# Kernel tuning notes

Hardware: AMD Instinct MI355X
Metric: run time of the kernel (lower is better)

## Reference

```python
import jax, jax.numpy as jnp
import numpy as np

B, T, C = 1, 4096, 1024   # batch, seq, n_embd
E, K = 64, 8              # num_experts, router top-k
G, TG = 8, 4              # n_group, topk_group
H, HS = 512, 2048         # expert hidden, shared-expert hidden
STD = 0.02


def setup_inputs() -> dict:
    key = jax.random.key(0)
    ks = jax.random.split(key, 9)
    return {
        "x": jax.random.normal(ks[0], (B, T, C), jnp.float32),
        "router_w": jax.random.normal(ks[1], (E, C), jnp.float32) * (C ** -0.5),
        "e_bias": jnp.zeros((E,), jnp.float32),  # e_score_correction_bias buffer
        "gate_w": jax.random.normal(ks[2], (E, C, H), jnp.float32) * STD,
        "up_w": jax.random.normal(ks[3], (E, C, H), jnp.float32) * STD,
        "down_w": jax.random.normal(ks[4], (E, H, C), jnp.float32) * STD,
        "sh_gate_w": jax.random.normal(ks[5], (C, HS), jnp.float32) * STD,
        "sh_up_w": jax.random.normal(ks[6], (C, HS), jnp.float32) * STD,
        "sh_down_w": jax.random.normal(ks[7], (HS, C), jnp.float32) * STD,
    }


def _route(xf, router_w, e_bias):
    # grouped sigmoid top-k routing with score-correction bias (group_limited_greedy)
    S = xf.shape[0]
    scores = jax.nn.sigmoid(xf @ router_w.T)          # [S,E], raw sigmoid scores
    sb = scores + e_bias                               # biased scores (selection only)
    epg = E // G
    # per-group score = sum of top (K // topk_group) biased scores in that group
    grp = jax.lax.top_k(sb.reshape(S, G, epg), K // TG)[0].sum(-1)   # [S,G]
    gidx = jax.lax.top_k(grp, TG)[1]                                 # [S,TG]
    gmask = jnp.zeros((S, G), bool).at[jnp.arange(S)[:, None], gidx].set(True)
    emask = jnp.repeat(gmask, epg, axis=1)                           # [S,E]
    masked = jnp.where(emask, sb, -jnp.inf)
    topk_idx = jax.lax.top_k(masked, K)[1]                           # [S,K]
    w = jnp.take_along_axis(scores, topk_idx, axis=1)                # raw scores gathered
    w = w / (w.sum(-1, keepdims=True) + 1e-20)                       # norm_topk_prob
    return topk_idx, w


def reference(x, router_w, e_bias, gate_w, up_w, down_w, sh_gate_w, sh_up_w, sh_down_w):
    Bq, Tq, Cq = x.shape
    xf = x.reshape(Bq * Tq, Cq)
    # always-on shared expert (SwiGLU)
    shared = (jax.nn.silu(xf @ sh_gate_w) * (xf @ sh_up_w)) @ sh_down_w
    topk_idx, w = _route(xf, router_w, e_bias)
    fe = topk_idx.reshape(-1)                          # [S*K] expert id per routed row
    order = jnp.argsort(fe, stable=True)               # sort rows by expert (grouped)
    tok = order // K                                   # source token of each sorted row
    sorted_x = xf[tok]                                 # [S*K, C]
    group_sizes = jnp.bincount(fe, length=E).astype(jnp.int32)
    # grouped GEMMs (== torch._grouped_mm / bmm-over-buckets in the original)
    g = jax.lax.ragged_dot(sorted_x, gate_w, group_sizes)
    u = jax.lax.ragged_dot(sorted_x, up_w, group_sizes)
    h = jax.nn.silu(g) * u
    o = jax.lax.ragged_dot(h, down_w, group_sizes)     # [S*K, C]
    o = o * w.reshape(-1)[order][:, None]              # weight by routing prob
    routed = jnp.zeros_like(xf).at[tok].add(o)         # combine back per token
    return (shared + routed).reshape(Bq, Tq, Cq)
```

## Files before the change

### kernel.cpp

```cpp
#include <hip/hip_runtime.h>
#include <hip/hip_bf16.h>
#include <stdint.h>


#define S_TOK 4096
#define C_DIM 1024
#define E_NUM 64
#define H_DIM 512
#define HS_DIM 2048
#define ROWS_TOTAL (S_TOK * 8)
#define T_TILES 320
#define NB_ROUTED_F (T_TILES * 8)
#define NB_SHARED_F (32 * 32)
#define NB_ROUTED_D (T_TILES * 8)
#define NB_SHARED_D (32 * 8)

typedef __attribute__((ext_vector_type(8))) short short8;
typedef __attribute__((ext_vector_type(4))) float f32x4;
typedef __attribute__((ext_vector_type(2))) unsigned int uint2v;

static __device__ __forceinline__ unsigned short f2bf(float f) {
    union { float f; uint32_t u; } v; v.f = f;
    uint32_t u = v.u;
    u += 0x7fffu + ((u >> 16) & 1u);
    return (unsigned short)(u >> 16);
}

static __device__ __forceinline__ void gl2lds16(const void* g, void* l) {
    __builtin_amdgcn_global_load_lds(
        (const __attribute__((address_space(1))) uint32_t*)g,
        (__attribute__((address_space(3))) uint32_t*)l, 16, 0, 0);
}

static __device__ __forceinline__ uint2v tr64(unsigned addr) {
    uint2v r;
    asm volatile("ds_read_b64_tr_b16 %0, %1" : "=v"(r) : "v"(addr));
    return r;
}

__global__ __launch_bounds__(256)
void router_scores_k(const float* __restrict__ x, const float* __restrict__ rw,
                     float* __restrict__ scores, int* __restrict__ counts) {
    if (blockIdx.x == 0 && threadIdx.x < E_NUM) counts[threadIdx.x] = 0;
    int t0 = blockIdx.x * 32;
    __shared__ float xs[32][36];
    __shared__ float wsm[64][36];
    int t = threadIdx.x;
    int tx = t & 15, ty = t >> 4;
    float acc[2][4] = {};
    for (int k0 = 0; k0 < C_DIM; k0 += 32) {
        {
            int r = t >> 3, c = t & 7;
            *(float4*)&xs[r][c * 4] = *(const float4*)(x + (size_t)(t0 + r) * C_DIM + k0 + c * 4);
        }
        #pragma unroll
        for (int i = 0; i < 2; i++) {
            int idx = t + 256 * i;
            int r = idx >> 3, c = idx & 7;
            *(float4*)&wsm[r][c * 4] = *(const float4*)(rw + (size_t)r * C_DIM + k0 + c * 4);
        }
        __syncthreads();
        #pragma unroll
        for (int kk = 0; kk < 32; kk += 4) {
            float4 a0 = *(const float4*)&xs[ty * 2 + 0][kk];
            float4 a1 = *(const float4*)&xs[ty * 2 + 1][kk];
            #pragma unroll
            for (int j = 0; j < 4; j++) {
                float4 b = *(const float4*)&wsm[tx * 4 + j][kk];
                acc[0][j] += a0.x * b.x + a0.y * b.y + a0.z * b.z + a0.w * b.w;
                acc[1][j] += a1.x * b.x + a1.y * b.y + a1.z * b.z + a1.w * b.w;
            }
        }
        __syncthreads();
    }
    #pragma unroll
    for (int i = 0; i < 2; i++)
        #pragma unroll
        for (int j = 0; j < 4; j++)
            scores[(size_t)(t0 + ty * 2 + i) * E_NUM + tx * 4 + j] =
                1.f / (1.f + __expf(-acc[i][j]));
}

__global__ __launch_bounds__(256)
void topk_k(const float* __restrict__ scores, const float* __restrict__ ebias,
            int* __restrict__ topk_idx, float* __restrict__ topk_w,
            int* __restrict__ counts) {
    int t = blockIdx.x * 4 + (threadIdx.x >> 6);
    int e = threadIdx.x & 63;
    float sc = scores[(size_t)t * E_NUM + e];
    float sb = sc + ebias[e];
    float m1 = sb, m2 = -1e30f;
    #pragma unroll
    for (int off = 1; off <= 4; off <<= 1) {
        float o1 = __shfl_xor(m1, off);
        float o2 = __shfl_xor(m2, off);
        float hi = fmaxf(m1, o1), lo = fminf(m1, o1);
        m2 = fmaxf(lo, fmaxf(m2, o2));
        m1 = hi;
    }
    float grp = m1 + m2;
    float grpv[8];
    #pragma unroll
    for (int g = 0; g < 8; g++) grpv[g] = __shfl(grp, g * 8);
    unsigned gsel = 0;
    #pragma unroll
    for (int k = 0; k < 4; k++) {
        float best = -1e30f; int bi = 0;
        #pragma unroll
        for (int g = 0; g < 8; g++)
            if (!((gsel >> g) & 1) && grpv[g] > best) { best = grpv[g]; bi = g; }
        gsel |= 1u << bi;
    }
    float val = ((gsel >> (e >> 3)) & 1) ? sb : -1e30f;
    int idx[8]; float sv[8]; float wsum = 0.f;
    #pragma unroll
    for (int k = 0; k < 8; k++) {
        uint32_t u = __float_as_uint(val);
        uint32_t mu = (u & 0x80000000u) ? ~u : (u | 0x80000000u);
        unsigned long long key = ((unsigned long long)mu << 6) | (unsigned long long)(63 - e);
        #pragma unroll
        for (int off = 32; off; off >>= 1) {
            unsigned long long ok = __shfl_xor(key, off);
            if (ok > key) key = ok;
        }
        int win = 63 - (int)(key & 63ull);
        idx[k] = win;
        sv[k] = __shfl(sc, win);
        wsum += sv[k];
        if (e == win) val = -1e30f;
    }
    float inv = 1.f / (wsum + 1e-20f);
    if (e < 8) {
        topk_idx[t * 8 + e] = idx[e];
        topk_w[t * 8 + e] = sv[e] * inv;
        atomicAdd(&counts[idx[e]], 1);
    }
}

__global__ void scan_k(const int* __restrict__ counts, int* __restrict__ base,
                       int* __restrict__ cursor, int* __restrict__ tile_e,
                       int* __restrict__ tile_m0) {
    int e = threadIdx.x;
    int c = counts[e];
    int s = c;
    #pragma unroll
    for (int off = 1; off < 64; off <<= 1) {
        int o = __shfl_up(s, off);
        if (e >= off) s += o;
    }
    int ex = s - c;
    base[e] = ex;
    cursor[e] = ex;
    int nt = (c + 127) >> 7;
    int ts = nt;
    #pragma unroll
    for (int off = 1; off < 64; off <<= 1) {
        int o = __shfl_up(ts, off);
        if (e >= off) ts += o;
    }
    int tb = ts - nt;
    for (int i = 0; i < nt; i++) { tile_e[tb + i] = e; tile_m0[tb + i] = i * 128; }
    int total = __shfl(ts, 63);
    for (int j = total + e; j < T_TILES; j += 64) tile_e[j] = -1;
}

__global__ void scatter_k(const int* __restrict__ topk_idx, const float* __restrict__ topk_w,
                          int* __restrict__ cursor, int* __restrict__ row_token,
                          float* __restrict__ row_wgt, int* __restrict__ pos_of) {
    int i = blockIdx.x * blockDim.x + threadIdx.x;
    int e = topk_idx[i];
    int pos = atomicAdd(&cursor[e], 1);
    row_token[pos] = i >> 3;
    row_wgt[pos] = topk_w[i];
    pos_of[i] = pos;
}

__global__ __launch_bounds__(256)
void combine_k(const float* __restrict__ O, const int* __restrict__ pos_of,
               float* __restrict__ out) {
    int t = blockIdx.x;
    int c = threadIdx.x;
    float4 s = ((const float4*)(out + (size_t)t * C_DIM))[c];
    int p[8];
    #pragma unroll
    for (int k = 0; k < 8; k++) p[k] = pos_of[t * 8 + k];
    #pragma unroll
    for (int k = 0; k < 8; k++) {
        float4 v = ((const float4*)(O + (size_t)p[k] * C_DIM))[c];
        s.x += v.x; s.y += v.y; s.z += v.z; s.w += v.w;
    }
    ((float4*)(out + (size_t)t * C_DIM))[c] = s;
}

__global__ __launch_bounds__(256)
void cvt_all_k(const float* __restrict__ i0, unsigned short* __restrict__ o0, int n0,
               const float* __restrict__ i1, unsigned short* __restrict__ o1, int n1,
               const float* __restrict__ i2, unsigned short* __restrict__ o2, int n2,
               const float* __restrict__ i3, unsigned short* __restrict__ o3, int n3,
               const float* __restrict__ i4, unsigned short* __restrict__ o4, int n4,
               const float* __restrict__ i5, unsigned short* __restrict__ o5, int n5,
               const float* __restrict__ i6, unsigned short* __restrict__ o6, int n6) {
    int g = blockIdx.x * 256 + threadIdx.x;
    const float* in; unsigned short* out;
    if (g < n0) { in = i0; out = o0; }
    else { g -= n0;
    if (g < n1) { in = i1; out = o1; }
    else { g -= n1;
    if (g < n2) { in = i2; out = o2; }
    else { g -= n2;
    if (g < n3) { in = i3; out = o3; }
    else { g -= n3;
    if (g < n4) { in = i4; out = o4; }
    else { g -= n4;
    if (g < n5) { in = i5; out = o5; }
    else { g -= n5;
    if (g >= n6) return;
    in = i6; out = o6; } } } } } }
    float4 v0 = ((const float4*)in)[2 * g];
    float4 v1 = ((const float4*)in)[2 * g + 1];
    unsigned short t[8] = { f2bf(v0.x), f2bf(v0.y), f2bf(v0.z), f2bf(v0.w),
                            f2bf(v1.x), f2bf(v1.y), f2bf(v1.z), f2bf(v1.w) };
    ((uint4*)out)[g] = *(uint4*)t;
}

__global__ __launch_bounds__(256, 3)
void fused_all_k(const short* __restrict__ xb,
                 const short* __restrict__ gate_b, const short* __restrict__ up_b,
                 const short* __restrict__ shg_b, const short* __restrict__ shu_b,
                 unsigned short* __restrict__ Hr, unsigned short* __restrict__ Hs,
                 const int* __restrict__ counts, const int* __restrict__ base,
                 const int* __restrict__ row_token,
                 const int* __restrict__ tile_e, const int* __restrict__ tile_m0) {
    constexpr int K = C_DIM;
    constexpr int NC = 4;
    constexpr int BS = 64 * 32;

    int bid = blockIdx.x;
    bool routed = bid < NB_ROUTED_F;
    const short* B1; const short* B2; unsigned short* Cout;
    int m0, n0, Mrows, rowbase, N;
    if (routed) {
        int ti = bid >> 3;
        int e = tile_e[ti];
        if (e < 0) return;
        m0 = tile_m0[ti]; n0 = (bid & 7) * 64;
        Mrows = counts[e]; rowbase = base[e];
        N = H_DIM;
        B1 = gate_b + (size_t)e * H_DIM * K;
        B2 = up_b   + (size_t)e * H_DIM * K;
        Cout = Hr;
    } else {
        int s = bid - NB_ROUTED_F;
        m0 = (s >> 5) * 128; n0 = (s & 31) * 64;
        Mrows = S_TOK; rowbase = 0;
        N = HS_DIM;
        B1 = shg_b; B2 = shu_b;
        Cout = Hs;
    }

    __shared__ short As[3 * 4096];
    __shared__ short Bs1[3 * BS / 2 * 2];
    __shared__ short Bs2[3 * 2048];

    int tid = threadIdx.x;
    int lane = tid & 63, w = tid >> 6;
    int wr = w >> 1, wc = w & 1;
    int quad = lane >> 4, l16 = lane & 15;
    int sr = lane >> 2, sc = lane & 3;

    const short* aptr[2];
    #pragma unroll
    for (int i = 0; i < 2; i++) {
        int row = w * 32 + i * 16 + sr;
        int mrow = m0 + row;
        int cl = mrow < Mrows ? mrow : (Mrows - 1);
        size_t arow = routed ? (size_t)row_token[rowbase + cl] : (size_t)cl;
        aptr[i] = xb + arow * K + sc * 8;
    }

    const short* b1ptr;
    const short* b2ptr;
    {
        int L = lane;
        int r = (L & 7) >> 1, c = (L & 1) * 8;
        int kc = w * 2 + (L >> 5);
        int nc = (L >> 3) & 3;
        b1ptr = B1 + (size_t)(kc * 4 + r) * N + n0 + nc * 16 + c;
        b2ptr = B2 + (size_t)(kc * 4 + r) * N + n0 + nc * 16 + c;
    }
    const size_t bstep = (size_t)32 * N;

    f32x4 acc1[4][2] = {};
    f32x4 acc2[4][2] = {};

    const int nk = K >> 5;
    auto stage = [&](int slot) {
        #pragma unroll
        for (int i = 0; i < 2; i++) {
            gl2lds16(aptr[i], &As[slot * 4096 + (w * 32 + i * 16) * 32]);
            aptr[i] += 32;
        }
        gl2lds16(b1ptr, &Bs1[slot * 2048 + w * 512]); b1ptr += bstep;
        gl2lds16(b2ptr, &Bs2[slot * 2048 + w * 512]); b2ptr += bstep;
    };
    stage(0);
    stage(1);

    unsigned trb1 = (unsigned)(size_t)&Bs1[0] + (unsigned)(quad * 2 * NC * 128 + l16 * 8);
    unsigned trb2 = (unsigned)(size_t)&Bs2[0] + (unsigned)(quad * 2 * NC * 128 + l16 * 8);
    auto rdB = [&](unsigned trb, int slot, int nb) -> short8 {
        unsigned a0 = trb + (unsigned)(slot * 4096 + nb * 128);
        uint2v lo = tr64(a0);
        uint2v hi = tr64(a0 + NC * 128);
        union { uint32_t u[4]; short8 s; } u;
        u.u[0] = lo[0]; u.u[1] = lo[1]; u.u[2] = hi[0]; u.u[3] = hi[1];
        return u.s;
    };

    int slot = 0, nslot = 2;
    for (int t = 0; t < nk; t++) {
        if (t + 1 < nk) {
            asm volatile("s_waitcnt vmcnt(4)" ::: "memory");
        } else {
            asm volatile("s_waitcnt vmcnt(0)" ::: "memory");
        }
        __builtin_amdgcn_s_barrier();
        __builtin_amdgcn_sched_barrier(0);

        if (t + 2 < nk) stage(nslot);

        short8 a[4], b1[2], b2[2];
        #pragma unroll
        for (int i = 0; i < 4; i++)
            a[i] = *(const short8*)&As[slot * 4096 + (wr * 64 + i * 16 + l16) * 32 + quad * 8];
        #pragma unroll
        for (int j = 0; j < 2; j++) {
            int nb = wc * 2 + j;
            b1[j] = rdB(trb1, slot, nb);
            b2[j] = rdB(trb2, slot, nb);
        }
        asm volatile("s_waitcnt lgkmcnt(0)" ::: "memory");
        __builtin_amdgcn_sched_barrier(0);
        #pragma unroll
        for (int i = 0; i < 4; i++)
            #pragma unroll
            for (int j = 0; j < 2; j++) {
                acc1[i][j] = __builtin_amdgcn_mfma_f32_16x16x32_bf16(a[i], b1[j], acc1[i][j], 0, 0, 0);
                acc2[i][j] = __builtin_amdgcn_mfma_f32_16x16x32_bf16(a[i], b2[j], acc2[i][j], 0, 0, 0);
            }
        slot = (slot == 2) ? 0 : slot + 1;
        nslot = (nslot == 2) ? 0 : nslot + 1;
    }

    #pragma unroll
    for (int i = 0; i < 4; i++) {
        #pragma unroll
        for (int rr = 0; rr < 4; rr++) {
            int row = m0 + wr * 64 + i * 16 + quad * 4 + rr;
            if (row >= Mrows) continue;
            size_t orow = (size_t)(rowbase + row);
            #pragma unroll
            for (int j = 0; j < 2; j++) {
                int n = n0 + wc * 32 + j * 16 + l16;
                float v = acc1[i][j][rr];
                float u = acc2[i][j][rr];
                float h = v / (1.f + __expf(-v)) * u;
                Cout[orow * N + n] = f2bf(h);
            }
        }
    }
}

__global__ __launch_bounds__(256, 3)
void down_all_k(const short* __restrict__ Hr, const short* __restrict__ Hs,
                const short* __restrict__ down_b, const short* __restrict__ shd_b,
                float* __restrict__ O, float* __restrict__ out,
                const int* __restrict__ counts, const int* __restrict__ base,
                const float* __restrict__ row_wgt,
                const int* __restrict__ tile_e, const int* __restrict__ tile_m0) {
    constexpr int N = C_DIM;
    constexpr int NC = 8;
    constexpr int BS = 128 * 32;

    int bid = blockIdx.x;
    bool routed = bid < NB_ROUTED_D;
    const short* A; const short* B1; float* Cout;
    int m0, n0, Mrows, rowbase, K;
    if (routed) {
        int ti = bid >> 3;
        int e = tile_e[ti];
        if (e < 0) return;
        m0 = tile_m0[ti]; n0 = (bid & 7) * 128;
        Mrows = counts[e]; rowbase = base[e];
        K = H_DIM;
        A = Hr;
        B1 = down_b + (size_t)e * N * H_DIM;
        Cout = O;
    } else {
        int s = bid - NB_ROUTED_D;
        m0 = (s >> 3) * 128; n0 = (s & 7) * 128;
        Mrows = S_TOK; rowbase = 0;
        K = HS_DIM;
        A = Hs;
        B1 = shd_b;
        Cout = out;
    }

    __shared__ short As[3 * 4096];
    __shared__ short Bs1[3 * BS];

    int tid = threadIdx.x;
    int lane = tid & 63, w = tid >> 6;
    int wr = w >> 1, wc = w & 1;
    int quad = lane >> 4, l16 = lane & 15;
    int sr = lane >> 2, sc = lane & 3;

    const short* aptr[2];
    #pragma unroll
    for (int i = 0; i < 2; i++) {
        int row = w * 32 + i * 16 + sr;
        int mrow = m0 + row;
        int cl = mrow < Mrows ? mrow : (Mrows - 1);
        aptr[i] = A + (size_t)(rowbase + cl) * K + sc * 8;
    }

    const short* b1ptr[2];
    {
        int L = lane;
        int r = (L & 7) >> 1, c = (L & 1) * 8;
        int nc = L >> 3;
        #pragma unroll
        for (int i = 0; i < 2; i++) {
            int kc = w * 2 + i;
            b1ptr[i] = B1 + (size_t)(kc * 4 + r) * N + n0 + nc * 16 + c;
        }
    }
    const size_t bstep = (size_t)32 * N;

    f32x4 acc1[4][4] = {};

    const int nk = K >> 5;
    auto stage = [&](int slot) {
        #pragma unroll
        for (int i = 0; i < 2; i++) {
            gl2lds16(aptr[i], &As[slot * 4096 + (w * 32 + i * 16) * 32]);
            aptr[i] += 32;
        }
        #pragma unroll
        for (int i = 0; i < 2; i++) {
            gl2lds16(b1ptr[i], &Bs1[slot * BS + (w * 2 + i) * 512]);
            b1ptr[i] += bstep;
        }
    };
    stage(0);
    stage(1);

    unsigned trb1 = (unsigned)(size_t)&Bs1[0] + (unsigned)(quad * 2 * NC * 128 + l16 * 8);
    auto rdB = [&](int slot, int nb) -> short8 {
        unsigned a0 = trb1 + (unsigned)(slot * BS * 2 + nb * 128);
        uint2v lo = tr64(a0);
        uint2v hi = tr64(a0 + NC * 128);
        union { uint32_t u[4]; short8 s; } u;
        u.u[0] = lo[0]; u.u[1] = lo[1]; u.u[2] = hi[0]; u.u[3] = hi[1];
        return u.s;
    };

    int slot = 0, nslot = 2;
    for (int t = 0; t < nk; t++) {
        if (t + 1 < nk) {
            asm volatile("s_waitcnt vmcnt(4)" ::: "memory");
        } else {
            asm volatile("s_waitcnt vmcnt(0)" ::: "memory");
        }
        __builtin_amdgcn_s_barrier();
        __builtin_amdgcn_sched_barrier(0);

        if (t + 2 < nk) stage(nslot);

        short8 a[4], b1[4];
        #pragma unroll
        for (int i = 0; i < 4; i++)
            a[i] = *(const short8*)&As[slot * 4096 + (wr * 64 + i * 16 + l16) * 32 + quad * 8];
        #pragma unroll
        for (int j = 0; j < 4; j++)
            b1[j] = rdB(slot, wc * 4 + j);
        asm volatile("s_waitcnt lgkmcnt(0)" ::: "memory");
        __builtin_amdgcn_sched_barrier(0);
        #pragma unroll
        for (int i = 0; i < 4; i++)
            #pragma unroll
            for (int j = 0; j < 4; j++)
                acc1[i][j] = __builtin_amdgcn_mfma_f32_16x16x32_bf16(a[i], b1[j], acc1[i][j], 0, 0, 0);
        slot = (slot == 2) ? 0 : slot + 1;
        nslot = (nslot == 2) ? 0 : nslot + 1;
    }

    #pragma unroll
    for (int i = 0; i < 4; i++) {
        #pragma unroll
        for (int rr = 0; rr < 4; rr++) {
            int row = m0 + wr * 64 + i * 16 + quad * 4 + rr;
            if (row >= Mrows) continue;
            size_t orow = (size_t)(rowbase + row);
            float scl = routed ? row_wgt[rowbase + row] : 1.f;
            #pragma unroll
            for (int j = 0; j < 4; j++) {
                int n = n0 + wc * 64 + j * 16 + l16;
                Cout[orow * N + n] = acc1[i][j][rr] * scl;
            }
        }
    }
}

extern "C" void kernel_launch(void* const* d_in, const int* in_sizes, int n_in,
                              void* d_out, int out_size, void* d_ws, size_t ws_size,
                              hipStream_t stream) {
    const float* x        = (const float*)d_in[0];
    const float* router_w = (const float*)d_in[1];
    const float* e_bias   = (const float*)d_in[2];
    const float* gate_w   = (const float*)d_in[3];
    const float* up_w     = (const float*)d_in[4];
    const float* down_w   = (const float*)d_in[5];
    const float* sh_gate  = (const float*)d_in[6];
    const float* sh_up    = (const float*)d_in[7];
    const float* sh_down  = (const float*)d_in[8];
    float* out = (float*)d_out;
    char* ws = (char*)d_ws;

    int*   counts    = (int*)(ws);
    int*   base      = (int*)(ws + 256);
    int*   cursor    = (int*)(ws + 512);
    int*   topk_idx  = (int*)(ws + 1024);
    float* topk_w    = (float*)(ws + 1024 + 131072);
    int*   row_token = (int*)(ws + 1024 + 2 * 131072);
    float* row_wgt   = (float*)(ws + 1024 + 3 * 131072);
    float* scoresbuf = (float*)(ws + 1024 + 4 * 131072);
    int*   pos_of    = (int*)(ws + 1664 * 1024);
    int*   tile_e    = (int*)(ws + 1800 * 1024);
    int*   tile_m0   = (int*)(ws + 1808 * 1024);
    const size_t MB = 1u << 20;
    unsigned short* xb        = (unsigned short*)(ws + 2 * MB);
    unsigned short* Hs        = (unsigned short*)(ws + 10 * MB);
    unsigned short* Hr        = (unsigned short*)(ws + 26 * MB);
    unsigned short* sh_gate_b = (unsigned short*)(ws + 58 * MB);
    unsigned short* sh_up_b   = (unsigned short*)(ws + 62 * MB);
    unsigned short* sh_down_b = (unsigned short*)(ws + 66 * MB);
    unsigned short* gate_b    = (unsigned short*)(ws + 70 * MB);
    unsigned short* up_b      = (unsigned short*)(ws + 134 * MB);
    unsigned short* down_b    = (unsigned short*)(ws + 198 * MB);
    float* O = (float*)(ws + 70 * MB);

    router_scores_k<<<S_TOK / 32, 256, 0, stream>>>(x, router_w, scoresbuf, counts);
    topk_k<<<S_TOK / 4, 256, 0, stream>>>(scoresbuf, e_bias, topk_idx, topk_w, counts);
    scan_k<<<1, 64, 0, stream>>>(counts, base, cursor, tile_e, tile_m0);
    scatter_k<<<ROWS_TOTAL / 256, 256, 0, stream>>>(topk_idx, topk_w, cursor, row_token, row_wgt, pos_of);

    const int NX = S_TOK * C_DIM / 8;
    const int NW = E_NUM * C_DIM * H_DIM / 8;
    const int NS = C_DIM * HS_DIM / 8;
    const int NTOT = NX + 3 * NW + 3 * NS;
    cvt_all_k<<<(NTOT + 255) / 256, 256, 0, stream>>>(
        x, xb, NX, gate_w, gate_b, NW, up_w, up_b, NW, down_w, down_b, NW,
        sh_gate, sh_gate_b, NS, sh_up, sh_up_b, NS, sh_down, sh_down_b, NS);

    fused_all_k<<<NB_ROUTED_F + NB_SHARED_F, 256, 0, stream>>>(
        (const short*)xb, (const short*)gate_b, (const short*)up_b,
        (const short*)sh_gate_b, (const short*)sh_up_b, Hr, Hs,
        counts, base, row_token, tile_e, tile_m0);

    down_all_k<<<NB_ROUTED_D + NB_SHARED_D, 256, 0, stream>>>(
        (const short*)Hr, (const short*)Hs, (const short*)down_b, (const short*)sh_down_b,
        O, out, counts, base, row_wgt, tile_e, tile_m0);

    combine_k<<<S_TOK, 256, 0, stream>>>(O, pos_of, out);
}
```

Baseline: 917.0 us.

## Double-buffer GEMM LDS, raise occupancy, pack bf16 conversion, reorder down blocks

Several changes land together. The up/gate and down GEMM kernels move from triple-buffered to double-buffered LDS, with the next stage issued before the wait and an extra barrier at the end of each iteration, and launch bounds go from 3 to 5 waves per SIMD. The fp32-to-bf16 conversion kernel now handles 16 elements per thread using the packed v_cvt_pk_bf16_f32 instruction. The down kernel now schedules the shared-expert blocks before the routed ones. The aim is more resident blocks and cheaper weight conversion, at the cost of shallower prefetch and an additional barrier per k-step.

Measured after the change: 1.272 ms. 1.39x slower.

```diff
diff --git a/kernel.cpp b/kernel.cpp
--- a/kernel.cpp
+++ b/kernel.cpp
@@ -24,6 +24,12 @@
     uint32_t u = v.u;
     u += 0x7fffu + ((u >> 16) & 1u);
     return (unsigned short)(u >> 16);
+}
+
+static __device__ __forceinline__ uint32_t cvtpk(float a, float b) {
+    uint32_t r;
+    asm("v_cvt_pk_bf16_f32 %0, %1, %2" : "=v"(r) : "v"(a), "v"(b));
+    return r;
 }
 
 static __device__ __forceinline__ void gl2lds16(const void* g, void* l) {
@@ -216,14 +222,20 @@
     else { g -= n5;
     if (g >= n6) return;
     in = i6; out = o6; } } } } } }
-    float4 v0 = ((const float4*)in)[2 * g];
-    float4 v1 = ((const float4*)in)[2 * g + 1];
-    unsigned short t[8] = { f2bf(v0.x), f2bf(v0.y), f2bf(v0.z), f2bf(v0.w),
-                            f2bf(v1.x), f2bf(v1.y), f2bf(v1.z), f2bf(v1.w) };
-    ((uint4*)out)[g] = *(uint4*)t;
-}
-
-__global__ __launch_bounds__(256, 3)
+    float4 v0 = ((const float4*)in)[4 * g];
+    float4 v1 = ((const float4*)in)[4 * g + 1];
+    float4 v2 = ((const float4*)in)[4 * g + 2];
+    float4 v3 = ((const float4*)in)[4 * g + 3];
+    uint32_t pk[8];
+    pk[0] = cvtpk(v0.x, v0.y); pk[1] = cvtpk(v0.z, v0.w);
+    pk[2] = cvtpk(v1.x, v1.y); pk[3] = cvtpk(v1.z, v1.w);
+    pk[4] = cvtpk(v2.x, v2.y); pk[5] = cvtpk(v2.z, v2.w);
+    pk[6] = cvtpk(v3.x, v3.y); pk[7] = cvtpk(v3.z, v3.w);
+    ((uint4*)out)[2 * g]     = *(uint4*)&pk[0];
+    ((uint4*)out)[2 * g + 1] = *(uint4*)&pk[4];
+}
+
+__global__ __launch_bounds__(256, 5)
 void fused_all_k(const short* __restrict__ xb,
                  const short* __restrict__ gate_b, const short* __restrict__ up_b,
                  const short* __restrict__ shg_b, const short* __restrict__ shu_b,
@@ -233,7 +245,6 @@
                  const int* __restrict__ tile_e, const int* __restrict__ tile_m0) {
     constexpr int K = C_DIM;
     constexpr int NC = 4;
-    constexpr int BS = 64 * 32;
 
     int bid = blockIdx.x;
     bool routed = bid < NB_ROUTED_F;
@@ -258,9 +269,9 @@
         Cout = Hs;
     }
 
-    __shared__ short As[3 * 4096];
-    __shared__ short Bs1[3 * BS / 2 * 2];
-    __shared__ short Bs2[3 * 2048];
+    __shared__ short As[2 * 4096];
+    __shared__ short Bs1[2 * 2048];
+    __shared__ short Bs2[2 * 2048];
 
     int tid = threadIdx.x;
     int lane = tid & 63, w = tid >> 6;
@@ -304,7 +315,6 @@
         gl2lds16(b2ptr, &Bs2[slot * 2048 + w * 512]); b2ptr += bstep;
     };
     stage(0);
-    stage(1);
 
     unsigned trb1 = (unsigned)(size_t)&Bs1[0] + (unsigned)(quad * 2 * NC * 128 + l16 * 8);
     unsigned trb2 = (unsigned)(size_t)&Bs2[0] + (unsigned)(quad * 2 * NC * 128 + l16 * 8);
@@ -317,17 +327,16 @@
         return u.s;
     };
 
-    int slot = 0, nslot = 2;
     for (int t = 0; t < nk; t++) {
+        int slot = t & 1;
         if (t + 1 < nk) {
+            stage(slot ^ 1);
             asm volatile("s_waitcnt vmcnt(4)" ::: "memory");
         } else {
             asm volatile("s_waitcnt vmcnt(0)" ::: "memory");
         }
         __builtin_amdgcn_s_barrier();
         __builtin_amdgcn_sched_barrier(0);
-
-        if (t + 2 < nk) stage(nslot);
 
         short8 a[4], b1[2], b2[2];
         #pragma unroll
@@ -348,8 +357,7 @@
                 acc1[i][j] = __builtin_amdgcn_mfma_f32_16x16x32_bf16(a[i], b1[j], acc1[i][j], 0, 0, 0);
                 acc2[i][j] = __builtin_amdgcn_mfma_f32_16x16x32_bf16(a[i], b2[j], acc2[i][j], 0, 0, 0);
             }
-        slot = (slot == 2) ? 0 : slot + 1;
-        nslot = (nslot == 2) ? 0 : nslot + 1;
+        if (t + 1 < nk) __builtin_amdgcn_s_barrier();
     }
 
     #pragma unroll
@@ -371,7 +379,7 @@
     }
 }
 
-__global__ __launch_bounds__(256, 3)
+__global__ __launch_bounds__(256, 5)
 void down_all_k(const short* __restrict__ Hr, const short* __restrict__ Hs,
                 const short* __restrict__ down_b, const short* __restrict__ shd_b,
                 float* __restrict__ O, float* __restrict__ out,
@@ -383,31 +391,31 @@
     constexpr int BS = 128 * 32;
 
     int bid = blockIdx.x;
-    bool routed = bid < NB_ROUTED_D;
+    bool shared_e = bid < NB_SHARED_D;
     const short* A; const short* B1; float* Cout;
     int m0, n0, Mrows, rowbase, K;
-    if (routed) {
-        int ti = bid >> 3;
+    if (shared_e) {
+        m0 = (bid >> 3) * 128; n0 = (bid & 7) * 128;
+        Mrows = S_TOK; rowbase = 0;
+        K = HS_DIM;
+        A = Hs;
+        B1 = shd_b;
+        Cout = out;
+    } else {
+        int rb = bid - NB_SHARED_D;
+        int ti = rb >> 3;
         int e = tile_e[ti];
         if (e < 0) return;
-        m0 = tile_m0[ti]; n0 = (bid & 7) * 128;
+        m0 = tile_m0[ti]; n0 = (rb & 7) * 128;
         Mrows = counts[e]; rowbase = base[e];
         K = H_DIM;
         A = Hr;
         B1 = down_b + (size_t)e * N * H_DIM;
         Cout = O;
-    } else {
-        int s = bid - NB_ROUTED_D;
-        m0 = (s >> 3) * 128; n0 = (s & 7) * 128;
-        Mrows = S_TOK; rowbase = 0;
-        K = HS_DIM;
-        A = Hs;
-        B1 = shd_b;
-        Cout = out;
-    }
-
-    __shared__ short As[3 * 4096];
-    __shared__ short Bs1[3 * BS];
+    }
+
+    __shared__ short As[2 * 4096];
+    __shared__ short Bs1[2 * BS];
 
     int tid = threadIdx.x;
     int lane = tid & 63, w = tid >> 6;
@@ -453,7 +461,6 @@
         }
     };
     stage(0);
-    stage(1);
 
     unsigned trb1 = (unsigned)(size_t)&Bs1[0] + (unsigned)(quad * 2 * NC * 128 + l16 * 8);
     auto rdB = [&](int slot, int nb) -> short8 {
@@ -465,17 +472,16 @@
         return u.s;
     };
 
-    int slot = 0, nslot = 2;
     for (int t = 0; t < nk; t++) {
+        int slot = t & 1;
         if (t + 1 < nk) {
+            stage(slot ^ 1);
             asm volatile("s_waitcnt vmcnt(4)" ::: "memory");
         } else {
             asm volatile("s_waitcnt vmcnt(0)" ::: "memory");
         }
         __builtin_amdgcn_s_barrier();
         __builtin_amdgcn_sched_barrier(0);
-
-        if (t + 2 < nk) stage(nslot);
 
         short8 a[4], b1[4];
         #pragma unroll
@@ -491,8 +497,7 @@
             #pragma unroll
             for (int j = 0; j < 4; j++)
                 acc1[i][j] = __builtin_amdgcn_mfma_f32_16x16x32_bf16(a[i], b1[j], acc1[i][j], 0, 0, 0);
-        slot = (slot == 2) ? 0 : slot + 1;
-        nslot = (nslot == 2) ? 0 : nslot + 1;
+        if (t + 1 < nk) __builtin_amdgcn_s_barrier();
     }
 
     #pragma unroll
@@ -502,7 +507,7 @@
             int row = m0 + wr * 64 + i * 16 + quad * 4 + rr;
             if (row >= Mrows) continue;
             size_t orow = (size_t)(rowbase + row);
-            float scl = routed ? row_wgt[rowbase + row] : 1.f;
+            float scl = shared_e ? 1.f : row_wgt[rowbase + row];
             #pragma unroll
             for (int j = 0; j < 4; j++) {
                 int n = n0 + wc * 64 + j * 16 + l16;
@@ -555,9 +560,9 @@
     scan_k<<<1, 64, 0, stream>>>(counts, base, cursor, tile_e, tile_m0);
     scatter_k<<<ROWS_TOTAL / 256, 256, 0, stream>>>(topk_idx, topk_w, cursor, row_token, row_wgt, pos_of);
 
-    const int NX = S_TOK * C_DIM / 8;
-    const int NW = E_NUM * C_DIM * H_DIM / 8;
-    const int NS = C_DIM * HS_DIM / 8;
+    const int NX = S_TOK * C_DIM / 16;
+    const int NW = E_NUM * C_DIM * H_DIM / 16;
+    const int NS = C_DIM * HS_DIM / 16;
     const int NTOT = NX + 3 * NW + 3 * NS;
     cvt_all_k<<<(NTOT + 255) / 256, 256, 0, stream>>>(
         x, xb, NX, gate_w, gate_b, NW, up_w, up_b, NW, down_w, down_b, NW,
@@ -568,7 +573,7 @@
         (const short*)sh_gate_b, (const short*)sh_up_b, Hr, Hs,
         counts, base, row_token, tile_e, tile_m0);
 
-    down_all_k<<<NB_ROUTED_D + NB_SHARED_D, 256, 0, stream>>>(
+    down_all_k<<<NB_SHARED_D + NB_ROUTED_D, 256, 0, stream>>>(
         (const short*)Hr, (const short*)Hs, (const short*)down_b, (const short*)sh_down_b,
         O, out, counts, base, row_wgt, tile_e, tile_m0);
 
```
